# Optimization experiments

Hardware: AMD Instinct MI355X
Metric: run time of the kernel (lower is better)

The kernel has to match this reference:

```python
import jax, jax.numpy as jnp
import numpy as np
from jax import lax

WIN = 9
EPS = 1e-05


def _box_sum(v, win):
    # v: [B, 1, D, H, W]
    pad = win // 2
    dn = lax.conv_dimension_numbers(v.shape, (1, 1, win, win, win), ('NCDHW', 'OIDHW', 'NCDHW'))
    k = jnp.ones((win,), v.dtype)
    # apply 1D sum along D, H, W in turn
    v = lax.conv_general_dilated(v, k.reshape(1, 1, win, 1, 1), (1, 1, 1), [(pad, pad), (0, 0), (0, 0)], dimension_numbers=dn)
    v = lax.conv_general_dilated(v, k.reshape(1, 1, 1, win, 1), (1, 1, 1), [(0, 0), (pad, pad), (0, 0)], dimension_numbers=dn)
    v = lax.conv_general_dilated(v, k.reshape(1, 1, 1, 1, win), (1, 1, 1), [(0, 0), (0, 0), (pad, pad)], dimension_numbers=dn)
    return v


def setup_inputs() -> dict:
    key = jax.random.key(0)
    k1, k2 = jax.random.split(key)
    shape = (2, 1, 160, 192, 160)
    x = jax.random.uniform(k1, shape, dtype=jnp.float32)
    y = jax.random.uniform(k2, shape, dtype=jnp.float32)
    return {"x": x, "y": y}


def reference(x, y):
    win = WIN
    win_size = float(win ** 3)
    x_sum = _box_sum(x, win)
    y_sum = _box_sum(y, win)
    x2_sum = _box_sum(x * x, win)
    y2_sum = _box_sum(y * y, win)
    xy_sum = _box_sum(x * y, win)
    cross = xy_sum - x_sum * y_sum / win_size
    x_var = jnp.maximum(x2_sum - x_sum * x_sum / win_size, EPS)
    y_var = jnp.maximum(y2_sum - y_sum * y_sum / win_size, EPS)
    cc = cross * cross / (x_var * y_var)
    return -jnp.mean(cc)
```

## Files before the change

### kernel.cpp

```cpp
#include <hip/hip_runtime.h>

#define BB 2
#define DD 160
#define HH 192
#define WW 160
#define HW (HH * WW)
#define PAD 4
#define TH 16
#define TW 16
#define EXT 24
#define XSTR 28
#define PLANE 768
#define WCS 456
#define WJS 28
#define HCS 272
#define HHS 17
#define CHUNK 28
#define NCH 6
#define NITER 36
#define WT (WW / TW)
#define HT (HH / TH)
#define NBLK (WT * HT * NCH * BB)
#define NTASK 288
#define EPS 1e-5f
#define INV_WS (1.0f / 729.0f)

__device__ __forceinline__ void bar_lgkm() {
  asm volatile("s_waitcnt lgkmcnt(0)" ::: "memory");
  __builtin_amdgcn_s_barrier();
  asm volatile("" ::: "memory");
}

__global__ void __launch_bounds__(256) k_lncc(
    const float* __restrict__ x, const float* __restrict__ y,
    float* __restrict__ partials)
{
  __shared__ __align__(16) float sbuf[2][PLANE];
  __shared__ __align__(16) float ones[32];
  __shared__ __align__(16) float wsum[5 * WCS];
  __shared__ __align__(16) float hsum[5 * HCS];
  __shared__ float red[4];

  const int t = threadIdx.x;
  const int w0 = blockIdx.x * TW;
  const int h0 = blockIdx.y * TH;
  const int bz = blockIdx.z;
  const int b = bz / NCH;
  const int chunk = bz - b * NCH;
  const int dc0 = chunk * CHUNK;
  const int g0 = dc0 - PAD;

  for (int i = t; i < 2 * PLANE; i += 256) (&sbuf[0][0])[i] = 0.f;
  if (t < 32) ones[t] = 1.0f;

  int la0, la1; bool tk0, tk1;
  const float* gp0; const float* gp1;
  {
    const float* bx = x + (long)b * DD * HW;
    const float* by = y + (long)b * DD * HW;
#define MKTASK(TAU, LA, TK, GP)                                           \
    {                                                                     \
      int tau = (TAU);                                                    \
      int a = tau / 144;                                                  \
      int rem = tau - 144 * a;                                            \
      int r = rem / 6;                                                    \
      int q = rem - 6 * r;                                                \
      int aa = (a < 2) ? a : 0;                                           \
      int gh = h0 - PAD + r;                                              \
      int gw = w0 - PAD + 4 * q;                                          \
      bool ok = (tau < NTASK) && ((unsigned)gh < (unsigned)HH) &&         \
                ((unsigned)gw < (unsigned)WW);                            \
      LA = aa * PLANE + r * XSTR + 4 * q;                                 \
      TK = ok;                                                            \
      GP = (aa ? by : bx) + (ok ? (gh * WW + gw) : 0);                    \
    }
    MKTASK(t, la0, tk0, gp0)
    MKTASK(256 + t, la1, tk1, gp1)
#undef MKTASK
  }

  const int c2 = t / 24, r2 = t - c2 * 24;
  const int arrA = ((c2 == 1) || (c2 == 3)) ? 1 : 0;
  const int arrB = (c2 == 2) ? 0 : 1;
  const bool useOnes = (c2 < 2);
  const int paOff = arrA * PLANE + r2 * XSTR;
  const int pbOff = arrB * PLANE + r2 * XSTR;
  float* const wwr = &wsum[c2 * WCS + r2];

  const int c3 = t / 16, w3 = t - c3 * 16;
  const float* const wrd = &wsum[c3 * WCS + w3 * WJS];
  float* const hwr = &hsum[c3 * HCS + w3];

  const int h4 = t >> 4, w4 = t & 15;
  const float* const hrd = &hsum[h4 * HHS + w4];

  float ring[9][5];
#pragma unroll
  for (int i = 0; i < 9; ++i)
#pragma unroll
    for (int c = 0; c < 5; ++c) ring[i][c] = 0.f;
  float run0 = 0.f, run1 = 0.f, run2 = 0.f, run3 = 0.f, run4 = 0.f, acc = 0.f;

  __syncthreads();

  float4 st0 = make_float4(0, 0, 0, 0), st1 = st0;
  bool ps0 = false, ps1 = false;
  {
    if ((unsigned)g0 < (unsigned)DD) {
      const long so = (long)g0 * HW;
      if (tk0) *(float4*)&sbuf[0][la0] = *(const float4*)(gp0 + so);
      if (tk1) *(float4*)&sbuf[0][la1] = *(const float4*)(gp1 + so);
    }
    const int g1i = g0 + 1;
    const bool v1 = ((unsigned)g1i < (unsigned)DD);
    const long so1 = (long)g1i * HW;
    ps0 = tk0 && v1; if (ps0) st0 = *(const float4*)(gp0 + so1);
    ps1 = tk1 && v1; if (ps1) st1 = *(const float4*)(gp1 + so1);
  }
  __syncthreads();

  for (int ko = 0; ko < 4; ++ko) {
#pragma unroll
    for (int jj = 0; jj < 9; ++jj) {
      const int k = ko * 9 + jj;
      const int g = g0 + k;
      const bool gv = ((unsigned)g < (unsigned)DD);

      if (gv && t < 120) {
        const float* pa = &sbuf[0][0] + paOff;
        const float* pb = useOnes ? &ones[0] : (&sbuf[0][0] + pbOff);
        float4 A0 = *(const float4*)(pa);
        float4 A1 = *(const float4*)(pa + 4);
        float4 A2 = *(const float4*)(pa + 8);
        float4 A3 = *(const float4*)(pa + 12);
        float4 A4 = *(const float4*)(pa + 16);
        float4 A5 = *(const float4*)(pa + 20);
        float4 B0 = *(const float4*)(pb);
        float4 B1 = *(const float4*)(pb + (useOnes ? 0 : 4));
        float4 B2 = *(const float4*)(pb + (useOnes ? 0 : 8));
        float4 B3 = *(const float4*)(pb + (useOnes ? 0 : 12));
        float4 B4 = *(const float4*)(pb + (useOnes ? 0 : 16));
        float4 B5 = *(const float4*)(pb + (useOnes ? 0 : 20));
        float q[EXT];
        q[0]=A0.x*B0.x; q[1]=A0.y*B0.y; q[2]=A0.z*B0.z; q[3]=A0.w*B0.w;
        q[4]=A1.x*B1.x; q[5]=A1.y*B1.y; q[6]=A1.z*B1.z; q[7]=A1.w*B1.w;
        q[8]=A2.x*B2.x; q[9]=A2.y*B2.y; q[10]=A2.z*B2.z; q[11]=A2.w*B2.w;
        q[12]=A3.x*B3.x; q[13]=A3.y*B3.y; q[14]=A3.z*B3.z; q[15]=A3.w*B3.w;
        q[16]=A4.x*B4.x; q[17]=A4.y*B4.y; q[18]=A4.z*B4.z; q[19]=A4.w*B4.w;
        q[20]=A5.x*B5.x; q[21]=A5.y*B5.y; q[22]=A5.z*B5.z; q[23]=A5.w*B5.w;
        float s = ((q[0] + q[1]) + (q[2] + q[3])) +
                  ((q[4] + q[5]) + (q[6] + q[7])) + q[8];
        wwr[0] = s;
#pragma unroll
        for (int j = 1; j < TW; ++j) {
          s += q[j + 8] - q[j - 1];
          wwr[j * WJS] = s;
        }
      }

      bar_lgkm();

      if (ps0) *(float4*)&sbuf[0][la0] = st0;
      if (ps1) *(float4*)&sbuf[0][la1] = st1;

      {
        const int gn = g + 2;
        const bool nv = (k + 2 < NITER) && ((unsigned)gn < (unsigned)DD);
        const long so = (long)gn * HW;
        ps0 = tk0 && nv; if (ps0) st0 = *(const float4*)(gp0 + so);
        ps1 = tk1 && nv; if (ps1) st1 = *(const float4*)(gp1 + so);
      }

      if (gv && t < 80) {
        float4 V0 = *(const float4*)(wrd);
        float4 V1 = *(const float4*)(wrd + 4);
        float4 V2 = *(const float4*)(wrd + 8);
        float4 V3 = *(const float4*)(wrd + 12);
        float4 V4 = *(const float4*)(wrd + 16);
        float4 V5 = *(const float4*)(wrd + 20);
        float v[EXT];
        v[0]=V0.x; v[1]=V0.y; v[2]=V0.z; v[3]=V0.w;
        v[4]=V1.x; v[5]=V1.y; v[6]=V1.z; v[7]=V1.w;
        v[8]=V2.x; v[9]=V2.y; v[10]=V2.z; v[11]=V2.w;
        v[12]=V3.x; v[13]=V3.y; v[14]=V3.z; v[15]=V3.w;
        v[16]=V4.x; v[17]=V4.y; v[18]=V4.z; v[19]=V4.w;
        v[20]=V5.x; v[21]=V5.y; v[22]=V5.z; v[23]=V5.w;
        float s = ((v[0] + v[1]) + (v[2] + v[3])) +
                  ((v[4] + v[5]) + (v[6] + v[7])) + v[8];
        hwr[0] = s;
#pragma unroll
        for (int h = 1; h < TH; ++h) {
          s += v[h + 8] - v[h - 1];
          hwr[h * HHS] = s;
        }
      }

      bar_lgkm();

      float hv0 = 0.f, hv1 = 0.f, hv2 = 0.f, hv3 = 0.f, hv4 = 0.f;
      if (gv) {
        hv0 = hrd[0];
        hv1 = hrd[HCS];
        hv2 = hrd[2 * HCS];
        hv3 = hrd[3 * HCS];
        hv4 = hrd[4 * HCS];
      }

      run0 += hv0 - ring[jj][0]; ring[jj][0] = hv0;
      run1 += hv1 - ring[jj][1]; ring[jj][1] = hv1;
      run2 += hv2 - ring[jj][2]; ring[jj][2] = hv2;
      run3 += hv3 - ring[jj][3]; ring[jj][3] = hv3;
      run4 += hv4 - ring[jj][4]; ring[jj][4] = hv4;

      if (k >= 8) {
        const int d = dc0 + (k - 8);
        if (d < DD) {
          float cross = fmaf(-run0 * INV_WS, run1, run4);
          float xv = fmaxf(fmaf(-run0 * INV_WS, run0, run2), EPS);
          float yv = fmaxf(fmaf(-run1 * INV_WS, run1, run3), EPS);
          acc += (cross * cross) * __builtin_amdgcn_rcpf(xv * yv);
        }
      }
    }
  }

#pragma unroll
  for (int o = 32; o > 0; o >>= 1) acc += __shfl_down(acc, o);
  if ((t & 63) == 0) red[t >> 6] = acc;
  __syncthreads();
  if (t == 0) {
    int bid = (bz * HT + blockIdx.y) * WT + blockIdx.x;
    partials[bid] = (red[0] + red[1]) + (red[2] + red[3]);
  }
}

__global__ void __launch_bounds__(256) k_finalize(
    const float* __restrict__ partials, float* __restrict__ out)
{
  __shared__ double red[256];
  double s = 0.0;
  for (int i = threadIdx.x; i < NBLK; i += 256) s += (double)partials[i];
  red[threadIdx.x] = s;
  __syncthreads();
  for (int o = 128; o > 0; o >>= 1) {
    if (threadIdx.x < o) red[threadIdx.x] += red[threadIdx.x + o];
    __syncthreads();
  }
  if (threadIdx.x == 0) {
    const double Nvox = (double)BB * DD * HH * WW;
    out[0] = (float)(-red[0] / Nvox);
  }
}

extern "C" void kernel_launch(void* const* d_in, const int* in_sizes, int n_in,
                              void* d_out, int out_size, void* d_ws, size_t ws_size,
                              hipStream_t stream) {
  (void)in_sizes; (void)n_in; (void)out_size; (void)ws_size;
  const float* x = (const float*)d_in[0];
  const float* y = (const float*)d_in[1];
  float* out = (float*)d_out;
  float* partials = (float*)d_ws;

  dim3 grid(WT, HT, BB * NCH);
  k_lncc<<<grid, 256, 0, stream>>>(x, y, partials);
  k_finalize<<<1, 256, 0, stream>>>(partials, out);
}
```

Measured before the change: 77.79 us.

## Shrink depth chunks to 19 planes and use tree-based window sums

Splits the depth axis into 9 chunks of 19 output planes instead of 6 chunks of 28. This raises the block count to fill more compute units, at the cost of more redundant halo-plane work per output (27 iterations per 19 planes versus 36 per 28). The W and H 9-tap box sums change from a serial sliding-window recurrence to a shared pairwise tree (pairs, quads, then combine). That removes the serial dependency chain and the add/subtract drift, but uses more registers and adds.

```diff
diff --git a/kernel.cpp b/kernel.cpp
--- a/kernel.cpp
+++ b/kernel.cpp
@@ -15,9 +15,9 @@
 #define WJS 28
 #define HCS 272
 #define HHS 17
-#define CHUNK 28
-#define NCH 6
-#define NITER 36
+#define CHUNK 19
+#define NCH 9
+#define NITER 27
 #define WT (WW / TW)
 #define HT (HH / TH)
 #define NBLK (WT * HT * NCH * BB)
@@ -119,7 +119,7 @@
   }
   __syncthreads();
 
-  for (int ko = 0; ko < 4; ++ko) {
+  for (int ko = 0; ko < 3; ++ko) {
 #pragma unroll
     for (int jj = 0; jj < 9; ++jj) {
       const int k = ko * 9 + jj;
@@ -148,14 +148,15 @@
         q[12]=A3.x*B3.x; q[13]=A3.y*B3.y; q[14]=A3.z*B3.z; q[15]=A3.w*B3.w;
         q[16]=A4.x*B4.x; q[17]=A4.y*B4.y; q[18]=A4.z*B4.z; q[19]=A4.w*B4.w;
         q[20]=A5.x*B5.x; q[21]=A5.y*B5.y; q[22]=A5.z*B5.z; q[23]=A5.w*B5.w;
-        float s = ((q[0] + q[1]) + (q[2] + q[3])) +
-                  ((q[4] + q[5]) + (q[6] + q[7])) + q[8];
-        wwr[0] = s;
-#pragma unroll
-        for (int j = 1; j < TW; ++j) {
-          s += q[j + 8] - q[j - 1];
-          wwr[j * WJS] = s;
-        }
+        float s2[23];
+#pragma unroll
+        for (int i = 0; i < 23; ++i) s2[i] = q[i] + q[i + 1];
+        float s4[21];
+#pragma unroll
+        for (int i = 0; i < 21; ++i) s4[i] = s2[i] + s2[i + 2];
+#pragma unroll
+        for (int j = 0; j < TW; ++j)
+          wwr[j * WJS] = (s4[j] + s4[j + 4]) + q[j + 8];
       }
 
       bar_lgkm();
@@ -185,14 +186,15 @@
         v[12]=V3.x; v[13]=V3.y; v[14]=V3.z; v[15]=V3.w;
         v[16]=V4.x; v[17]=V4.y; v[18]=V4.z; v[19]=V4.w;
         v[20]=V5.x; v[21]=V5.y; v[22]=V5.z; v[23]=V5.w;
-        float s = ((v[0] + v[1]) + (v[2] + v[3])) +
-                  ((v[4] + v[5]) + (v[6] + v[7])) + v[8];
-        hwr[0] = s;
-#pragma unroll
-        for (int h = 1; h < TH; ++h) {
-          s += v[h + 8] - v[h - 1];
-          hwr[h * HHS] = s;
-        }
+        float u2[23];
+#pragma unroll
+        for (int i = 0; i < 23; ++i) u2[i] = v[i] + v[i + 1];
+        float u4[21];
+#pragma unroll
+        for (int i = 0; i < 21; ++i) u4[i] = u2[i] + u2[i + 2];
+#pragma unroll
+        for (int h = 0; h < TH; ++h)
+          hwr[h * HHS] = (u4[h] + u4[h + 4]) + v[h + 8];
       }
 
       bar_lgkm();
```

Result: slower. 94.33 us (+21.3%).

## Software-pipeline W-pass and H-pass across warps with double-buffered wsum

Applied to the files above, without the earlier changes.

The W-direction box-sum for plane m+1 (threads 0-127) now runs concurrently with the H-direction pass for plane m (threads 128-207), using a double-buffered wsum array. Before, these two stages ran one after the other inside each iteration with a barrier between them. A prologue computes the first W-pass, and the loop still has two barriers per step, placed differently. This adds LDS footprint and a second barrier and relies on warp specialization to overlap the two stages.

```diff
diff --git a/kernel.cpp b/kernel.cpp
--- a/kernel.cpp
+++ b/kernel.cpp
@@ -13,6 +13,7 @@
 #define PLANE 768
 #define WCS 456
 #define WJS 28
+#define WPS (5 * WCS)
 #define HCS 272
 #define HHS 17
 #define CHUNK 28
@@ -37,7 +38,7 @@
 {
   __shared__ __align__(16) float sbuf[2][PLANE];
   __shared__ __align__(16) float ones[32];
-  __shared__ __align__(16) float wsum[5 * WCS];
+  __shared__ __align__(16) float wsum[2 * WPS];
   __shared__ __align__(16) float hsum[5 * HCS];
   __shared__ float red[4];
 
@@ -85,10 +86,11 @@
   const bool useOnes = (c2 < 2);
   const int paOff = arrA * PLANE + r2 * XSTR;
   const int pbOff = arrB * PLANE + r2 * XSTR;
-  float* const wwr = &wsum[c2 * WCS + r2];
-
-  const int c3 = t / 16, w3 = t - c3 * 16;
-  const float* const wrd = &wsum[c3 * WCS + w3 * WJS];
+  const int wwOff = c2 * WCS + r2;
+
+  const int tt = t - 128;
+  const int c3 = (tt >= 0 ? tt : 0) / 16, w3 = (tt >= 0 ? tt : 0) & 15;
+  const int wrOff = c3 * WCS + w3 * WJS;
   float* const hwr = &hsum[c3 * HCS + w3];
 
   const int h4 = t >> 4, w4 = t & 15;
@@ -102,14 +104,48 @@
   float run0 = 0.f, run1 = 0.f, run2 = 0.f, run3 = 0.f, run4 = 0.f, acc = 0.f;
 
   __syncthreads();
+
+#define P2_BODY(PARBASE)                                                   \
+  {                                                                        \
+    const float* pa = &sbuf[0][0] + paOff;                                 \
+    const float* pb = useOnes ? &ones[0] : (&sbuf[0][0] + pbOff);          \
+    float4 A0 = *(const float4*)(pa);                                      \
+    float4 A1 = *(const float4*)(pa + 4);                                  \
+    float4 A2 = *(const float4*)(pa + 8);                                  \
+    float4 A3 = *(const float4*)(pa + 12);                                 \
+    float4 A4 = *(const float4*)(pa + 16);                                 \
+    float4 A5 = *(const float4*)(pa + 20);                                 \
+    float4 B0 = *(const float4*)(pb);                                      \
+    float4 B1 = *(const float4*)(pb + (useOnes ? 0 : 4));                  \
+    float4 B2 = *(const float4*)(pb + (useOnes ? 0 : 8));                  \
+    float4 B3 = *(const float4*)(pb + (useOnes ? 0 : 12));                 \
+    float4 B4 = *(const float4*)(pb + (useOnes ? 0 : 16));                 \
+    float4 B5 = *(const float4*)(pb + (useOnes ? 0 : 20));                 \
+    float q[EXT];                                                          \
+    q[0]=A0.x*B0.x; q[1]=A0.y*B0.y; q[2]=A0.z*B0.z; q[3]=A0.w*B0.w;        \
+    q[4]=A1.x*B1.x; q[5]=A1.y*B1.y; q[6]=A1.z*B1.z; q[7]=A1.w*B1.w;        \
+    q[8]=A2.x*B2.x; q[9]=A2.y*B2.y; q[10]=A2.z*B2.z; q[11]=A2.w*B2.w;      \
+    q[12]=A3.x*B3.x; q[13]=A3.y*B3.y; q[14]=A3.z*B3.z; q[15]=A3.w*B3.w;    \
+    q[16]=A4.x*B4.x; q[17]=A4.y*B4.y; q[18]=A4.z*B4.z; q[19]=A4.w*B4.w;    \
+    q[20]=A5.x*B5.x; q[21]=A5.y*B5.y; q[22]=A5.z*B5.z; q[23]=A5.w*B5.w;    \
+    float s = ((q[0] + q[1]) + (q[2] + q[3])) +                            \
+              ((q[4] + q[5]) + (q[6] + q[7])) + q[8];                      \
+    float* wq = &wsum[(PARBASE) + wwOff];                                  \
+    wq[0] = s;                                                             \
+    _Pragma("unroll")                                                      \
+    for (int j = 1; j < TW; ++j) {                                         \
+      s += q[j + 8] - q[j - 1];                                            \
+      wq[j * WJS] = s;                                                     \
+    }                                                                      \
+  }
 
   float4 st0 = make_float4(0, 0, 0, 0), st1 = st0;
   bool ps0 = false, ps1 = false;
   {
     if ((unsigned)g0 < (unsigned)DD) {
       const long so = (long)g0 * HW;
-      if (tk0) *(float4*)&sbuf[0][la0] = *(const float4*)(gp0 + so);
-      if (tk1) *(float4*)&sbuf[0][la1] = *(const float4*)(gp1 + so);
+      if (tk0) *(float4*)&(&sbuf[0][0])[la0] = *(const float4*)(gp0 + so);
+      if (tk1) *(float4*)&(&sbuf[0][0])[la1] = *(const float4*)(gp1 + so);
     }
     const int g1i = g0 + 1;
     const bool v1 = ((unsigned)g1i < (unsigned)DD);
@@ -118,93 +154,74 @@
     ps1 = tk1 && v1; if (ps1) st1 = *(const float4*)(gp1 + so1);
   }
   __syncthreads();
+  if (((unsigned)g0 < (unsigned)DD) && t < 120) P2_BODY(0)
+  bar_lgkm();
+  if (ps0) *(float4*)&(&sbuf[0][0])[la0] = st0;
+  if (ps1) *(float4*)&(&sbuf[0][0])[la1] = st1;
+  {
+    const int gn = g0 + 2;
+    const bool nv = (2 < NITER) && ((unsigned)gn < (unsigned)DD);
+    const long so = (long)gn * HW;
+    ps0 = tk0 && nv; if (ps0) st0 = *(const float4*)(gp0 + so);
+    ps1 = tk1 && nv; if (ps1) st1 = *(const float4*)(gp1 + so);
+  }
+  bar_lgkm();
 
   for (int ko = 0; ko < 4; ++ko) {
 #pragma unroll
     for (int jj = 0; jj < 9; ++jj) {
-      const int k = ko * 9 + jj;
-      const int g = g0 + k;
-      const bool gv = ((unsigned)g < (unsigned)DD);
-
-      if (gv && t < 120) {
-        const float* pa = &sbuf[0][0] + paOff;
-        const float* pb = useOnes ? &ones[0] : (&sbuf[0][0] + pbOff);
-        float4 A0 = *(const float4*)(pa);
-        float4 A1 = *(const float4*)(pa + 4);
-        float4 A2 = *(const float4*)(pa + 8);
-        float4 A3 = *(const float4*)(pa + 12);
-        float4 A4 = *(const float4*)(pa + 16);
-        float4 A5 = *(const float4*)(pa + 20);
-        float4 B0 = *(const float4*)(pb);
-        float4 B1 = *(const float4*)(pb + (useOnes ? 0 : 4));
-        float4 B2 = *(const float4*)(pb + (useOnes ? 0 : 8));
-        float4 B3 = *(const float4*)(pb + (useOnes ? 0 : 12));
-        float4 B4 = *(const float4*)(pb + (useOnes ? 0 : 16));
-        float4 B5 = *(const float4*)(pb + (useOnes ? 0 : 20));
-        float q[EXT];
-        q[0]=A0.x*B0.x; q[1]=A0.y*B0.y; q[2]=A0.z*B0.z; q[3]=A0.w*B0.w;
-        q[4]=A1.x*B1.x; q[5]=A1.y*B1.y; q[6]=A1.z*B1.z; q[7]=A1.w*B1.w;
-        q[8]=A2.x*B2.x; q[9]=A2.y*B2.y; q[10]=A2.z*B2.z; q[11]=A2.w*B2.w;
-        q[12]=A3.x*B3.x; q[13]=A3.y*B3.y; q[14]=A3.z*B3.z; q[15]=A3.w*B3.w;
-        q[16]=A4.x*B4.x; q[17]=A4.y*B4.y; q[18]=A4.z*B4.z; q[19]=A4.w*B4.w;
-        q[20]=A5.x*B5.x; q[21]=A5.y*B5.y; q[22]=A5.z*B5.z; q[23]=A5.w*B5.w;
-        float s = ((q[0] + q[1]) + (q[2] + q[3])) +
-                  ((q[4] + q[5]) + (q[6] + q[7])) + q[8];
-        wwr[0] = s;
-#pragma unroll
-        for (int j = 1; j < TW; ++j) {
-          s += q[j + 8] - q[j - 1];
-          wwr[j * WJS] = s;
+      const int m = ko * 9 + jj + 1;
+      const int s = m - 1;
+
+      if (t < 128) {
+        if ((m < NITER) && ((unsigned)(g0 + m) < (unsigned)DD) && (t < 120))
+          P2_BODY((m & 1) * WPS)
+      } else {
+        if (((unsigned)(g0 + s) < (unsigned)DD) && (tt < 80)) {
+          const float* wrd = &wsum[(s & 1) * WPS + wrOff];
+          float4 V0 = *(const float4*)(wrd);
+          float4 V1 = *(const float4*)(wrd + 4);
+          float4 V2 = *(const float4*)(wrd + 8);
+          float4 V3 = *(const float4*)(wrd + 12);
+          float4 V4 = *(const float4*)(wrd + 16);
+          float4 V5 = *(const float4*)(wrd + 20);
+          float v[EXT];
+          v[0]=V0.x; v[1]=V0.y; v[2]=V0.z; v[3]=V0.w;
+          v[4]=V1.x; v[5]=V1.y; v[6]=V1.z; v[7]=V1.w;
+          v[8]=V2.x; v[9]=V2.y; v[10]=V2.z; v[11]=V2.w;
+          v[12]=V3.x; v[13]=V3.y; v[14]=V3.z; v[15]=V3.w;
+          v[16]=V4.x; v[17]=V4.y; v[18]=V4.z; v[19]=V4.w;
+          v[20]=V5.x; v[21]=V5.y; v[22]=V5.z; v[23]=V5.w;
+          float sv = ((v[0] + v[1]) + (v[2] + v[3])) +
+                     ((v[4] + v[5]) + (v[6] + v[7])) + v[8];
+          hwr[0] = sv;
+#pragma unroll
+          for (int h = 1; h < TH; ++h) {
+            sv += v[h + 8] - v[h - 1];
+            hwr[h * HHS] = sv;
+          }
         }
       }
 
       bar_lgkm();
 
-      if (ps0) *(float4*)&sbuf[0][la0] = st0;
-      if (ps1) *(float4*)&sbuf[0][la1] = st1;
-
-      {
-        const int gn = g + 2;
-        const bool nv = (k + 2 < NITER) && ((unsigned)gn < (unsigned)DD);
-        const long so = (long)gn * HW;
-        ps0 = tk0 && nv; if (ps0) st0 = *(const float4*)(gp0 + so);
-        ps1 = tk1 && nv; if (ps1) st1 = *(const float4*)(gp1 + so);
-      }
-
-      if (gv && t < 80) {
-        float4 V0 = *(const float4*)(wrd);
-        float4 V1 = *(const float4*)(wrd + 4);
-        float4 V2 = *(const float4*)(wrd + 8);
-        float4 V3 = *(const float4*)(wrd + 12);
-        float4 V4 = *(const float4*)(wrd + 16);
-        float4 V5 = *(const float4*)(wrd + 20);
-        float v[EXT];
-        v[0]=V0.x; v[1]=V0.y; v[2]=V0.z; v[3]=V0.w;
-        v[4]=V1.x; v[5]=V1.y; v[6]=V1.z; v[7]=V1.w;
-        v[8]=V2.x; v[9]=V2.y; v[10]=V2.z; v[11]=V2.w;
-        v[12]=V3.x; v[13]=V3.y; v[14]=V3.z; v[15]=V3.w;
-        v[16]=V4.x; v[17]=V4.y; v[18]=V4.z; v[19]=V4.w;
-        v[20]=V5.x; v[21]=V5.y; v[22]=V5.z; v[23]=V5.w;
-        float s = ((v[0] + v[1]) + (v[2] + v[3])) +
-                  ((v[4] + v[5]) + (v[6] + v[7])) + v[8];
-        hwr[0] = s;
-#pragma unroll
-        for (int h = 1; h < TH; ++h) {
-          s += v[h + 8] - v[h - 1];
-          hwr[h * HHS] = s;
-        }
-      }
-
-      bar_lgkm();
-
       float hv0 = 0.f, hv1 = 0.f, hv2 = 0.f, hv3 = 0.f, hv4 = 0.f;
-      if (gv) {
+      if ((unsigned)(g0 + s) < (unsigned)DD) {
         hv0 = hrd[0];
         hv1 = hrd[HCS];
         hv2 = hrd[2 * HCS];
         hv3 = hrd[3 * HCS];
         hv4 = hrd[4 * HCS];
       }
+      if (ps0) *(float4*)&(&sbuf[0][0])[la0] = st0;
+      if (ps1) *(float4*)&(&sbuf[0][0])[la1] = st1;
+      {
+        const int gn = g0 + m + 2;
+        const bool nv = (m + 2 < NITER) && ((unsigned)gn < (unsigned)DD);
+        const long so = (long)gn * HW;
+        ps0 = tk0 && nv; if (ps0) st0 = *(const float4*)(gp0 + so);
+        ps1 = tk1 && nv; if (ps1) st1 = *(const float4*)(gp1 + so);
+      }
 
       run0 += hv0 - ring[jj][0]; ring[jj][0] = hv0;
       run1 += hv1 - ring[jj][1]; ring[jj][1] = hv1;
@@ -212,8 +229,8 @@
       run3 += hv3 - ring[jj][3]; ring[jj][3] = hv3;
       run4 += hv4 - ring[jj][4]; ring[jj][4] = hv4;
 
-      if (k >= 8) {
-        const int d = dc0 + (k - 8);
+      if (s >= 8) {
+        const int d = dc0 + (s - 8);
         if (d < DD) {
           float cross = fmaf(-run0 * INV_WS, run1, run4);
           float xv = fmaxf(fmaf(-run0 * INV_WS, run0, run2), EPS);
@@ -221,6 +238,8 @@
           acc += (cross * cross) * __builtin_amdgcn_rcpf(xv * yv);
         }
       }
+
+      bar_lgkm();
     }
   }
 
```

New measurement: 76.16 us. -2.1%, faster.
